# Optimization experiments

Measured on AMD Instinct MI355X. Metric: run time of the kernel, lower is better.

## Reference

```python
import jax, jax.numpy as jnp
import numpy as np

NEG_BIG = -9e15  # matches torch's -9000000000000000.0 mask value
ALPHA = 0.2      # LeakyReLU negative slope


def setup_inputs() -> dict:
    key = jax.random.key(0)
    k1, k2, k3 = jax.random.split(key, 3)
    B, N, Fin, Fout = 8, 2048, 64, 64
    h = jax.random.normal(k1, (B, N, Fin), dtype=jnp.float32)
    adj = jax.random.randint(k2, (B, N, N), 0, 2, dtype=jnp.int32)
    kW, ka = jax.random.split(k3)
    # xavier_uniform with gain=1.414
    gW = 1.414 * np.sqrt(6.0 / (Fin + Fout))
    W = jax.random.uniform(kW, (Fin, Fout), minval=-gW, maxval=gW, dtype=jnp.float32)
    ga = 1.414 * np.sqrt(6.0 / (2 * Fout + 1))
    a = jax.random.uniform(ka, (2 * Fout, 1), minval=-ga, maxval=ga, dtype=jnp.float32)
    return {"h": h, "adj": adj, "W": W, "a": a}


def reference(h, adj, W, a):
    # Wh: [B, N, Fout]
    Wh = jnp.einsum("bnf,fo->bno", h, W)
    Fout = W.shape[1]
    a1 = a[:Fout, 0]   # source part of attention vector
    a2 = a[Fout:, 0]   # target part
    # e_ij = leakyrelu(a1.Wh_i + a2.Wh_j) -- rank-1 decomposition of the
    # repeat/cat construction; avoids the [B,N,N,2F] intermediate.
    s = Wh @ a1        # [B, N]
    t = Wh @ a2        # [B, N]
    e = s[:, :, None] + t[:, None, :]            # [B, N, N]
    e = jnp.where(e > 0, e, ALPHA * e)           # LeakyReLU
    e = jnp.where(adj > 0, e, NEG_BIG)           # adjacency mask
    attention = jax.nn.softmax(e, axis=2)
    # dropout omitted: reference is eval-mode (F.dropout is identity when not training)
    h_prime = jnp.einsum("bij,bjo->bio", attention, Wh)
    return jax.nn.elu(h_prime)                   # concat=True branch
```

## Files before the change

kernel.cpp:

```cpp
#include <hip/hip_runtime.h>


#define ALPHA 0.2f

typedef __attribute__((ext_vector_type(8))) short  short8;
typedef __attribute__((ext_vector_type(4))) float  f32x4;

static __device__ __forceinline__ unsigned short f2bf(float f) {
    unsigned u = __builtin_bit_cast(unsigned, f);
    u += 0x7fffu + ((u >> 16) & 1u);
    return (unsigned short)(u >> 16);
}

static __device__ __forceinline__ unsigned pack_bf2(float lo, float hi) {
    unsigned ulo = __builtin_bit_cast(unsigned, lo) + 0x8000u;
    unsigned uhi = __builtin_bit_cast(unsigned, hi) + 0x8000u;
    return __builtin_amdgcn_perm(uhi, ulo, 0x07060302);
}

__global__ __launch_bounds__(256) void k01(
    const float* __restrict__ h, const int* __restrict__ adj,
    const float* __restrict__ W, const float* __restrict__ a,
    uint4* __restrict__ whF, float* __restrict__ sw,
    float* __restrict__ tw, unsigned char* __restrict__ mask)
{
    __shared__ float W_l[64 * 65];
    __shared__ float wa[128];
    __shared__ float tile[4 * 16 * 65];

    const int tid = threadIdx.x;

    if (blockIdx.x >= 256) {
        const int mb = blockIdx.x - 256;
        const int4* a4 = (const int4*)adj;
        #pragma unroll 1
        for (int g0 = 0; g0 < 16; g0 += 4) {
            int4 v0a, v0b, v1a, v1b, v2a, v2b, v3a, v3b;
            const size_t p0 = (size_t)mb * 4096 + (size_t)g0 * 256 + tid;
            v0a = a4[p0 * 2];          v0b = a4[p0 * 2 + 1];
            v1a = a4[(p0 + 256) * 2];  v1b = a4[(p0 + 256) * 2 + 1];
            v2a = a4[(p0 + 512) * 2];  v2b = a4[(p0 + 512) * 2 + 1];
            v3a = a4[(p0 + 768) * 2];  v3b = a4[(p0 + 768) * 2 + 1];
            unsigned b0 = (v0a.x ? 1u:0u)|(v0a.y ? 2u:0u)|(v0a.z ? 4u:0u)|(v0a.w ? 8u:0u)
                        | (v0b.x ?16u:0u)|(v0b.y ?32u:0u)|(v0b.z ?64u:0u)|(v0b.w ?128u:0u);
            unsigned b1 = (v1a.x ? 1u:0u)|(v1a.y ? 2u:0u)|(v1a.z ? 4u:0u)|(v1a.w ? 8u:0u)
                        | (v1b.x ?16u:0u)|(v1b.y ?32u:0u)|(v1b.z ?64u:0u)|(v1b.w ?128u:0u);
            unsigned b2 = (v2a.x ? 1u:0u)|(v2a.y ? 2u:0u)|(v2a.z ? 4u:0u)|(v2a.w ? 8u:0u)
                        | (v2b.x ?16u:0u)|(v2b.y ?32u:0u)|(v2b.z ?64u:0u)|(v2b.w ?128u:0u);
            unsigned b3 = (v3a.x ? 1u:0u)|(v3a.y ? 2u:0u)|(v3a.z ? 4u:0u)|(v3a.w ? 8u:0u)
                        | (v3b.x ?16u:0u)|(v3b.y ?32u:0u)|(v3b.z ?64u:0u)|(v3b.w ?128u:0u);
            mask[p0]       = (unsigned char)b0;
            mask[p0 + 256] = (unsigned char)b1;
            mask[p0 + 512] = (unsigned char)b2;
            mask[p0 + 768] = (unsigned char)b3;
        }
        return;
    }

    const int lane = tid & 63, wv = tid >> 6;
    const int im   = lane & 15, kq = lane >> 4;

    #pragma unroll
    for (int k = 0; k < 16; ++k) {
        int e = tid + 256 * k;
        W_l[(e >> 6) * 65 + (e & 63)] = W[e];
    }
    __syncthreads();

    if (tid < 128) {
        int f = tid & 63;
        const float* ap = a + (tid >> 6) * 64;
        float acc = 0.f;
        #pragma unroll 8
        for (int o = 0; o < 64; ++o) acc += W_l[f * 65 + o] * ap[o];
        wa[tid] = acc;
    }
    __syncthreads();

    short8 bf[4][2];
    #pragma unroll
    for (int nb = 0; nb < 4; ++nb)
        #pragma unroll
        for (int ks = 0; ks < 2; ++ks)
            #pragma unroll
            for (int u = 0; u < 8; ++u)
                bf[nb][ks][u] = (short)f2bf(W_l[(ks * 32 + kq * 8 + u) * 65 + nb * 16 + im]);

    const int row0 = blockIdx.x * 64 + wv * 16;
    const float* hrow = h + (size_t)(row0 + im) * 64;

    float hv[2][8];
    short8 af[2];
    float sp = 0.f, tp = 0.f;
    #pragma unroll
    for (int ks = 0; ks < 2; ++ks) {
        float4 A = *(const float4*)(hrow + ks * 32 + kq * 8);
        float4 Bv = *(const float4*)(hrow + ks * 32 + kq * 8 + 4);
        hv[ks][0] = A.x;  hv[ks][1] = A.y;  hv[ks][2] = A.z;  hv[ks][3] = A.w;
        hv[ks][4] = Bv.x; hv[ks][5] = Bv.y; hv[ks][6] = Bv.z; hv[ks][7] = Bv.w;
        #pragma unroll
        for (int u = 0; u < 8; ++u) {
            int f = ks * 32 + kq * 8 + u;
            sp += hv[ks][u] * wa[f];
            tp += hv[ks][u] * wa[64 + f];
            af[ks][u] = (short)f2bf(hv[ks][u]);
        }
    }
    sp += __shfl_xor(sp, 16, 64); sp += __shfl_xor(sp, 32, 64);
    tp += __shfl_xor(tp, 16, 64); tp += __shfl_xor(tp, 32, 64);
    if (lane < 16) {
        sw[row0 + lane] = sp;
        tw[row0 + lane] = tp;
    }

    f32x4 acc[4] = {{0.f,0.f,0.f,0.f},{0.f,0.f,0.f,0.f},{0.f,0.f,0.f,0.f},{0.f,0.f,0.f,0.f}};
    #pragma unroll
    for (int ks = 0; ks < 2; ++ks)
        #pragma unroll
        for (int nb = 0; nb < 4; ++nb)
            acc[nb] = __builtin_amdgcn_mfma_f32_16x16x32_bf16(af[ks], bf[nb][ks], acc[nb], 0, 0, 0);

    #pragma unroll
    for (int nb = 0; nb < 4; ++nb)
        #pragma unroll
        for (int r = 0; r < 4; ++r)
            tile[wv * 1040 + (kq * 4 + r) * 65 + nb * 16 + im] = acc[nb][r];
    __syncthreads();

    {
        const int blk_row0 = blockIdx.x * 64;
        const int bb2 = blk_row0 >> 11;
        const int c_base = (blk_row0 & 2047) >> 5;
        #pragma unroll
        for (int k = 0; k < 2; ++k) {
            int e = tid + 256 * k;
            int l = e & 63, ot = (e >> 6) & 3, cl_ = e >> 8;
            int o = ot * 16 + (l & 15);
            int jb = cl_ * 32 + (l >> 4) * 8;
            unsigned d0, d1, d2, d3;
            {
                int j0 = jb;
                d0 = pack_bf2(tile[(j0 >> 4) * 1040 + (j0 & 15) * 65 + o],
                              tile[(j0 >> 4) * 1040 + ((j0 & 15) + 1) * 65 + o]);
                j0 = jb + 2;
                d1 = pack_bf2(tile[(j0 >> 4) * 1040 + (j0 & 15) * 65 + o],
                              tile[(j0 >> 4) * 1040 + ((j0 & 15) + 1) * 65 + o]);
                j0 = jb + 4;
                d2 = pack_bf2(tile[(j0 >> 4) * 1040 + (j0 & 15) * 65 + o],
                              tile[(j0 >> 4) * 1040 + ((j0 & 15) + 1) * 65 + o]);
                j0 = jb + 6;
                d3 = pack_bf2(tile[(j0 >> 4) * 1040 + (j0 & 15) * 65 + o],
                              tile[(j0 >> 4) * 1040 + ((j0 & 15) + 1) * 65 + o]);
            }
            uint4 val = {d0, d1, d2, d3};
            whF[(size_t)(((bb2 * 64 + c_base + cl_) * 4 + ot)) * 64 + l] = val;
        }
    }
}

__global__ __launch_bounds__(256, 2) void k2_attn(
    const unsigned* __restrict__ mask, const uint4* __restrict__ whF,
    const float* __restrict__ sw, const float* __restrict__ tw,
    float* __restrict__ out)
{
    __shared__ float eB[2048];
    __shared__ float eD[2048];
    __shared__ float cpart[4 * 2176];

    const int tid  = threadIdx.x;
    const int lane = tid & 63, wv = tid >> 6;
    const int im   = lane & 15, kq = lane >> 4;
    const int b    = blockIdx.x >> 6;
    const int i0   = (blockIdx.x & 63) << 5;

    {
        const float4* tp4 = (const float4*)(tw + (size_t)b * 2048);
        float4 t0 = tp4[tid], t1 = tp4[tid + 256];
        float4 e0 = {__expf(t0.x), __expf(t0.y), __expf(t0.z), __expf(t0.w)};
        float4 e1 = {__expf(t1.x), __expf(t1.y), __expf(t1.z), __expf(t1.w)};
        float4 f0 = {__expf(ALPHA*t0.x), __expf(ALPHA*t0.y), __expf(ALPHA*t0.z), __expf(ALPHA*t0.w)};
        float4 f1 = {__expf(ALPHA*t1.x), __expf(ALPHA*t1.y), __expf(ALPHA*t1.z), __expf(ALPHA*t1.w)};
        *(float4*)&eB[tid * 4] = e0;  *(float4*)&eB[(tid + 256) * 4] = e1;
        *(float4*)&eD[tid * 4] = f0;  *(float4*)&eD[(tid + 256) * 4] = f1;
    }

    const uint4* mr0 = (const uint4*)(mask + (size_t)(b * 2048 + i0 + im) * 64 + wv * 16);
    const uint4* mr1 = (const uint4*)(mask + (size_t)(b * 2048 + i0 + 16 + im) * 64 + wv * 16);
    const uint4 mA0 = mr0[0], mB0 = mr0[1], mC0 = mr0[2], mD0 = mr0[3];
    const uint4 mA1 = mr1[0], mB1 = mr1[1], mC1 = mr1[2], mD1 = mr1[3];
    const unsigned mm0[16] = {mA0.x, mA0.y, mA0.z, mA0.w, mB0.x, mB0.y, mB0.z, mB0.w,
                              mC0.x, mC0.y, mC0.z, mC0.w, mD0.x, mD0.y, mD0.z, mD0.w};
    const unsigned mm1[16] = {mA1.x, mA1.y, mA1.z, mA1.w, mB1.x, mB1.y, mB1.z, mB1.w,
                              mC1.x, mC1.y, mC1.z, mC1.w, mD1.x, mD1.y, mD1.z, mD1.w};

    const float sl0 = sw[b * 2048 + i0 + im];
    const float sl1 = sw[b * 2048 + i0 + 16 + im];
    const float al0 = __expf(sl0), cl0 = __expf(ALPHA * sl0);
    const float al1 = __expf(sl1), cl1 = __expf(ALPHA * sl1);

    const int j00 = wv * 512 + kq * 8;
    const uint4* wbase = whF + (size_t)((b * 64 + wv * 16) * 4) * 64 + lane;

    short8 onesf;
    {
        const short ov = (im == 0) ? (short)0x3F80 : (short)0;
        #pragma unroll
        for (int u = 0; u < 8; ++u) onesf[u] = ov;
    }

    __syncthreads();

    f32x4 acc0 = {0.f,0.f,0.f,0.f}, acc1 = {0.f,0.f,0.f,0.f};
    f32x4 acc2 = {0.f,0.f,0.f,0.f}, acc3 = {0.f,0.f,0.f,0.f};
    f32x4 acc4 = {0.f,0.f,0.f,0.f}, acc5 = {0.f,0.f,0.f,0.f};
    f32x4 acc6 = {0.f,0.f,0.f,0.f}, acc7 = {0.f,0.f,0.f,0.f};
    f32x4 az0  = {0.f,0.f,0.f,0.f}, az1  = {0.f,0.f,0.f,0.f};

    #pragma unroll
    for (int s = 0; s < 16; ++s) {
        const uint4 w0 = wbase[(s * 4 + 0) * 64];
        const uint4 w1 = wbase[(s * 4 + 1) * 64];
        const uint4 w2 = wbase[(s * 4 + 2) * 64];
        const uint4 w3 = wbase[(s * 4 + 3) * 64];

        const float4 bA  = *(const float4*)&eB[j00 + s * 32];
        const float4 bBv = *(const float4*)&eB[j00 + s * 32 + 4];
        const float4 dA  = *(const float4*)&eD[j00 + s * 32];
        const float4 dBv = *(const float4*)&eD[j00 + s * 32 + 4];
        const unsigned mb0 = (mm0[s] >> (kq * 8)) & 0xffu;
        const unsigned mb1 = (mm1[s] >> (kq * 8)) & 0xffu;

        float p0 = fmaxf(al0 * bA.x,  cl0 * dA.x);   p0 = (mb0 &   1u) ? p0 : 0.f;
        float p1 = fmaxf(al0 * bA.y,  cl0 * dA.y);   p1 = (mb0 &   2u) ? p1 : 0.f;
        float p2 = fmaxf(al0 * bA.z,  cl0 * dA.z);   p2 = (mb0 &   4u) ? p2 : 0.f;
        float p3 = fmaxf(al0 * bA.w,  cl0 * dA.w);   p3 = (mb0 &   8u) ? p3 : 0.f;
        float p4 = fmaxf(al0 * bBv.x, cl0 * dBv.x);  p4 = (mb0 &  16u) ? p4 : 0.f;
        float p5 = fmaxf(al0 * bBv.y, cl0 * dBv.y);  p5 = (mb0 &  32u) ? p5 : 0.f;
        float p6 = fmaxf(al0 * bBv.z, cl0 * dBv.z);  p6 = (mb0 &  64u) ? p6 : 0.f;
        float p7 = fmaxf(al0 * bBv.w, cl0 * dBv.w);  p7 = (mb0 & 128u) ? p7 : 0.f;

        int4 ai0;
        ai0.x = (int)pack_bf2(p0, p1);
        ai0.y = (int)pack_bf2(p2, p3);
        ai0.z = (int)pack_bf2(p4, p5);
        ai0.w = (int)pack_bf2(p6, p7);
        const short8 af0 = __builtin_bit_cast(short8, ai0);

        float q0 = fmaxf(al1 * bA.x,  cl1 * dA.x);   q0 = (mb1 &   1u) ? q0 : 0.f;
        float q1 = fmaxf(al1 * bA.y,  cl1 * dA.y);   q1 = (mb1 &   2u) ? q1 : 0.f;
        float q2 = fmaxf(al1 * bA.z,  cl1 * dA.z);   q2 = (mb1 &   4u) ? q2 : 0.f;
        float q3 = fmaxf(al1 * bA.w,  cl1 * dA.w);   q3 = (mb1 &   8u) ? q3 : 0.f;
        float q4 = fmaxf(al1 * bBv.x, cl1 * dBv.x);  q4 = (mb1 &  16u) ? q4 : 0.f;
        float q5 = fmaxf(al1 * bBv.y, cl1 * dBv.y);  q5 = (mb1 &  32u) ? q5 : 0.f;
        float q6 = fmaxf(al1 * bBv.z, cl1 * dBv.z);  q6 = (mb1 &  64u) ? q6 : 0.f;
        float q7 = fmaxf(al1 * bBv.w, cl1 * dBv.w);  q7 = (mb1 & 128u) ? q7 : 0.f;

        int4 ai1;
        ai1.x = (int)pack_bf2(q0, q1);
        ai1.y = (int)pack_bf2(q2, q3);
        ai1.z = (int)pack_bf2(q4, q5);
        ai1.w = (int)pack_bf2(q6, q7);
        const short8 af1 = __builtin_bit_cast(short8, ai1);

        acc0 = __builtin_amdgcn_mfma_f32_16x16x32_bf16(af0, __builtin_bit_cast(short8, w0), acc0, 0, 0, 0);
        acc1 = __builtin_amdgcn_mfma_f32_16x16x32_bf16(af0, __builtin_bit_cast(short8, w1), acc1, 0, 0, 0);
        acc2 = __builtin_amdgcn_mfma_f32_16x16x32_bf16(af0, __builtin_bit_cast(short8, w2), acc2, 0, 0, 0);
        acc3 = __builtin_amdgcn_mfma_f32_16x16x32_bf16(af0, __builtin_bit_cast(short8, w3), acc3, 0, 0, 0);
        az0  = __builtin_amdgcn_mfma_f32_16x16x32_bf16(af0, onesf, az0, 0, 0, 0);

        acc4 = __builtin_amdgcn_mfma_f32_16x16x32_bf16(af1, __builtin_bit_cast(short8, w0), acc4, 0, 0, 0);
        acc5 = __builtin_amdgcn_mfma_f32_16x16x32_bf16(af1, __builtin_bit_cast(short8, w1), acc5, 0, 0, 0);
        acc6 = __builtin_amdgcn_mfma_f32_16x16x32_bf16(af1, __builtin_bit_cast(short8, w2), acc6, 0, 0, 0);
        acc7 = __builtin_amdgcn_mfma_f32_16x16x32_bf16(af1, __builtin_bit_cast(short8, w3), acc7, 0, 0, 0);
        az1  = __builtin_amdgcn_mfma_f32_16x16x32_bf16(af1, onesf, az1, 0, 0, 0);
    }

    #pragma unroll
    for (int r = 0; r < 4; ++r) {
        const int row = kq * 4 + r;
        float* cp0 = &cpart[wv * 2176 + row * 68];
        cp0[ 0 + im] = acc0[r];
        cp0[16 + im] = acc1[r];
        cp0[32 + im] = acc2[r];
        cp0[48 + im] = acc3[r];
        float* cp1 = &cpart[wv * 2176 + (16 + row) * 68];
        cp1[ 0 + im] = acc4[r];
        cp1[16 + im] = acc5[r];
        cp1[32 + im] = acc6[r];
        cp1[48 + im] = acc7[r];
        if (im == 0) { cp0[64] = az0[r]; cp1[64] = az1[r]; }
    }
    __syncthreads();

    #pragma unroll
    for (int k = 0; k < 2; ++k) {
        const int idx4 = tid + 256 * k;
        const int i  = idx4 >> 4;
        const int oc = (idx4 & 15) << 2;
        const float4 s0 = *(const float4*)&cpart[0 * 2176 + i * 68 + oc];
        const float4 s1 = *(const float4*)&cpart[1 * 2176 + i * 68 + oc];
        const float4 s2 = *(const float4*)&cpart[2 * 2176 + i * 68 + oc];
        const float4 s3 = *(const float4*)&cpart[3 * 2176 + i * 68 + oc];
        float z = cpart[0 * 2176 + i * 68 + 64] + cpart[1 * 2176 + i * 68 + 64]
                + cpart[2 * 2176 + i * 68 + 64] + cpart[3 * 2176 + i * 68 + 64];
        if (z == 0.f) z = 1.f;
        const float inv = 1.f / z;
        float4 rv;
        rv.x = ((s0.x + s1.x) + (s2.x + s3.x)) * inv;
        rv.y = ((s0.y + s1.y) + (s2.y + s3.y)) * inv;
        rv.z = ((s0.z + s1.z) + (s2.z + s3.z)) * inv;
        rv.w = ((s0.w + s1.w) + (s2.w + s3.w)) * inv;
        rv.x = rv.x > 0.f ? rv.x : expm1f(rv.x);
        rv.y = rv.y > 0.f ? rv.y : expm1f(rv.y);
        rv.z = rv.z > 0.f ? rv.z : expm1f(rv.z);
        rv.w = rv.w > 0.f ? rv.w : expm1f(rv.w);
        *(float4*)(out + ((size_t)(b * 2048 + i0 + i)) * 64 + oc) = rv;
    }
}

extern "C" void kernel_launch(void* const* d_in, const int* in_sizes, int n_in,
                              void* d_out, int out_size, void* d_ws, size_t ws_size,
                              hipStream_t stream) {
    const float* h   = (const float*)d_in[0];
    const int*   adj = (const int*)d_in[1];
    const float* W   = (const float*)d_in[2];
    const float* a   = (const float*)d_in[3];
    float* out = (float*)d_out;

    uint4* whF = (uint4*)d_ws;
    float* sw  = (float*)((char*)d_ws + 2097152);
    float* tw  = (float*)((char*)d_ws + 2097152 + 65536);
    unsigned char* mask = (unsigned char*)((char*)d_ws + 2097152 + 131072);

    hipLaunchKernelGGL(k01, dim3(1280), dim3(256), 0, stream, h, adj, W, a, whF, sw, tw, mask);
    hipLaunchKernelGGL(k2_attn, dim3(512), dim3(256), 0, stream,
                       (const unsigned*)mask, whF, sw, tw, out);
}
```

Measured before the change: 212.8 us.

## Read int32 adjacency directly in attention kernel, drop bitmask pre-pass

Removes the adjacency-to-bitmask compaction blocks from the first kernel, so it now only computes Wh, s and t. The attention kernel loads the int32 adjacency rows itself inside its main loop and uses them as the softmax mask. This drops the write and re-read of the intermediate bitmask and the extra blocks in the first launch. The cost is that the large adjacency read now happens inside the occupancy-limited attention kernel, with less coalesced 32-byte-per-lane row accesses. That could add memory latency to the compute loop.

Result: faster. 204.5 us (-3.9%).

```diff
diff --git a/kernel.cpp b/kernel.cpp
--- a/kernel.cpp
+++ b/kernel.cpp
@@ -18,45 +18,16 @@
     return __builtin_amdgcn_perm(uhi, ulo, 0x07060302);
 }
 
-__global__ __launch_bounds__(256) void k01(
-    const float* __restrict__ h, const int* __restrict__ adj,
-    const float* __restrict__ W, const float* __restrict__ a,
-    uint4* __restrict__ whF, float* __restrict__ sw,
-    float* __restrict__ tw, unsigned char* __restrict__ mask)
+__global__ __launch_bounds__(256) void k1(
+    const float* __restrict__ h, const float* __restrict__ W,
+    const float* __restrict__ a, uint4* __restrict__ whF,
+    float* __restrict__ sw, float* __restrict__ tw)
 {
     __shared__ float W_l[64 * 65];
     __shared__ float wa[128];
     __shared__ float tile[4 * 16 * 65];
 
     const int tid = threadIdx.x;
-
-    if (blockIdx.x >= 256) {
-        const int mb = blockIdx.x - 256;
-        const int4* a4 = (const int4*)adj;
-        #pragma unroll 1
-        for (int g0 = 0; g0 < 16; g0 += 4) {
-            int4 v0a, v0b, v1a, v1b, v2a, v2b, v3a, v3b;
-            const size_t p0 = (size_t)mb * 4096 + (size_t)g0 * 256 + tid;
-            v0a = a4[p0 * 2];          v0b = a4[p0 * 2 + 1];
-            v1a = a4[(p0 + 256) * 2];  v1b = a4[(p0 + 256) * 2 + 1];
-            v2a = a4[(p0 + 512) * 2];  v2b = a4[(p0 + 512) * 2 + 1];
-            v3a = a4[(p0 + 768) * 2];  v3b = a4[(p0 + 768) * 2 + 1];
-            unsigned b0 = (v0a.x ? 1u:0u)|(v0a.y ? 2u:0u)|(v0a.z ? 4u:0u)|(v0a.w ? 8u:0u)
-                        | (v0b.x ?16u:0u)|(v0b.y ?32u:0u)|(v0b.z ?64u:0u)|(v0b.w ?128u:0u);
-            unsigned b1 = (v1a.x ? 1u:0u)|(v1a.y ? 2u:0u)|(v1a.z ? 4u:0u)|(v1a.w ? 8u:0u)
-                        | (v1b.x ?16u:0u)|(v1b.y ?32u:0u)|(v1b.z ?64u:0u)|(v1b.w ?128u:0u);
-            unsigned b2 = (v2a.x ? 1u:0u)|(v2a.y ? 2u:0u)|(v2a.z ? 4u:0u)|(v2a.w ? 8u:0u)
-                        | (v2b.x ?16u:0u)|(v2b.y ?32u:0u)|(v2b.z ?64u:0u)|(v2b.w ?128u:0u);
-            unsigned b3 = (v3a.x ? 1u:0u)|(v3a.y ? 2u:0u)|(v3a.z ? 4u:0u)|(v3a.w ? 8u:0u)
-                        | (v3b.x ?16u:0u)|(v3b.y ?32u:0u)|(v3b.z ?64u:0u)|(v3b.w ?128u:0u);
-            mask[p0]       = (unsigned char)b0;
-            mask[p0 + 256] = (unsigned char)b1;
-            mask[p0 + 512] = (unsigned char)b2;
-            mask[p0 + 768] = (unsigned char)b3;
-        }
-        return;
-    }
-
     const int lane = tid & 63, wv = tid >> 6;
     const int im   = lane & 15, kq = lane >> 4;
 
@@ -159,7 +130,7 @@
 }
 
 __global__ __launch_bounds__(256, 2) void k2_attn(
-    const unsigned* __restrict__ mask, const uint4* __restrict__ whF,
+    const int* __restrict__ adj, const uint4* __restrict__ whF,
     const float* __restrict__ sw, const float* __restrict__ tw,
     float* __restrict__ out)
 {
@@ -184,21 +155,15 @@
         *(float4*)&eD[tid * 4] = f0;  *(float4*)&eD[(tid + 256) * 4] = f1;
     }
 
-    const uint4* mr0 = (const uint4*)(mask + (size_t)(b * 2048 + i0 + im) * 64 + wv * 16);
-    const uint4* mr1 = (const uint4*)(mask + (size_t)(b * 2048 + i0 + 16 + im) * 64 + wv * 16);
-    const uint4 mA0 = mr0[0], mB0 = mr0[1], mC0 = mr0[2], mD0 = mr0[3];
-    const uint4 mA1 = mr1[0], mB1 = mr1[1], mC1 = mr1[2], mD1 = mr1[3];
-    const unsigned mm0[16] = {mA0.x, mA0.y, mA0.z, mA0.w, mB0.x, mB0.y, mB0.z, mB0.w,
-                              mC0.x, mC0.y, mC0.z, mC0.w, mD0.x, mD0.y, mD0.z, mD0.w};
-    const unsigned mm1[16] = {mA1.x, mA1.y, mA1.z, mA1.w, mB1.x, mB1.y, mB1.z, mB1.w,
-                              mC1.x, mC1.y, mC1.z, mC1.w, mD1.x, mD1.y, mD1.z, mD1.w};
+    const int j00 = wv * 512 + kq * 8;
+    const int4* arow0 = (const int4*)(adj + (size_t)(b * 2048 + i0 + im) * 2048) + (j00 >> 2);
+    const int4* arow1 = (const int4*)(adj + (size_t)(b * 2048 + i0 + 16 + im) * 2048) + (j00 >> 2);
 
     const float sl0 = sw[b * 2048 + i0 + im];
     const float sl1 = sw[b * 2048 + i0 + 16 + im];
     const float al0 = __expf(sl0), cl0 = __expf(ALPHA * sl0);
     const float al1 = __expf(sl1), cl1 = __expf(ALPHA * sl1);
 
-    const int j00 = wv * 512 + kq * 8;
     const uint4* wbase = whF + (size_t)((b * 64 + wv * 16) * 4) * 64 + lane;
 
     short8 onesf;
@@ -223,21 +188,24 @@
         const uint4 w2 = wbase[(s * 4 + 2) * 64];
         const uint4 w3 = wbase[(s * 4 + 3) * 64];
 
+        const int4 a0A = arow0[s * 8];
+        const int4 a0B = arow0[s * 8 + 1];
+        const int4 a1A = arow1[s * 8];
+        const int4 a1B = arow1[s * 8 + 1];
+
         const float4 bA  = *(const float4*)&eB[j00 + s * 32];
         const float4 bBv = *(const float4*)&eB[j00 + s * 32 + 4];
         const float4 dA  = *(const float4*)&eD[j00 + s * 32];
         const float4 dBv = *(const float4*)&eD[j00 + s * 32 + 4];
-        const unsigned mb0 = (mm0[s] >> (kq * 8)) & 0xffu;
-        const unsigned mb1 = (mm1[s] >> (kq * 8)) & 0xffu;
-
-        float p0 = fmaxf(al0 * bA.x,  cl0 * dA.x);   p0 = (mb0 &   1u) ? p0 : 0.f;
-        float p1 = fmaxf(al0 * bA.y,  cl0 * dA.y);   p1 = (mb0 &   2u) ? p1 : 0.f;
-        float p2 = fmaxf(al0 * bA.z,  cl0 * dA.z);   p2 = (mb0 &   4u) ? p2 : 0.f;
-        float p3 = fmaxf(al0 * bA.w,  cl0 * dA.w);   p3 = (mb0 &   8u) ? p3 : 0.f;
-        float p4 = fmaxf(al0 * bBv.x, cl0 * dBv.x);  p4 = (mb0 &  16u) ? p4 : 0.f;
-        float p5 = fmaxf(al0 * bBv.y, cl0 * dBv.y);  p5 = (mb0 &  32u) ? p5 : 0.f;
-        float p6 = fmaxf(al0 * bBv.z, cl0 * dBv.z);  p6 = (mb0 &  64u) ? p6 : 0.f;
-        float p7 = fmaxf(al0 * bBv.w, cl0 * dBv.w);  p7 = (mb0 & 128u) ? p7 : 0.f;
+
+        float p0 = fmaxf(al0 * bA.x,  cl0 * dA.x);   p0 = a0A.x ? p0 : 0.f;
+        float p1 = fmaxf(al0 * bA.y,  cl0 * dA.y);   p1 = a0A.y ? p1 : 0.f;
+        float p2 = fmaxf(al0 * bA.z,  cl0 * dA.z);   p2 = a0A.z ? p2 : 0.f;
+        float p3 = fmaxf(al0 * bA.w,  cl0 * dA.w);   p3 = a0A.w ? p3 : 0.f;
+        float p4 = fmaxf(al0 * bBv.x, cl0 * dBv.x);  p4 = a0B.x ? p4 : 0.f;
+        float p5 = fmaxf(al0 * bBv.y, cl0 * dBv.y);  p5 = a0B.y ? p5 : 0.f;
+        float p6 = fmaxf(al0 * bBv.z, cl0 * dBv.z);  p6 = a0B.z ? p6 : 0.f;
+        float p7 = fmaxf(al0 * bBv.w, cl0 * dBv.w);  p7 = a0B.w ? p7 : 0.f;
 
         int4 ai0;
         ai0.x = (int)pack_bf2(p0, p1);
@@ -246,14 +214,14 @@
         ai0.w = (int)pack_bf2(p6, p7);
         const short8 af0 = __builtin_bit_cast(short8, ai0);
 
-        float q0 = fmaxf(al1 * bA.x,  cl1 * dA.x);   q0 = (mb1 &   1u) ? q0 : 0.f;
-        float q1 = fmaxf(al1 * bA.y,  cl1 * dA.y);   q1 = (mb1 &   2u) ? q1 : 0.f;
-        float q2 = fmaxf(al1 * bA.z,  cl1 * dA.z);   q2 = (mb1 &   4u) ? q2 : 0.f;
-        float q3 = fmaxf(al1 * bA.w,  cl1 * dA.w);   q3 = (mb1 &   8u) ? q3 : 0.f;
-        float q4 = fmaxf(al1 * bBv.x, cl1 * dBv.x);  q4 = (mb1 &  16u) ? q4 : 0.f;
-        float q5 = fmaxf(al1 * bBv.y, cl1 * dBv.y);  q5 = (mb1 &  32u) ? q5 : 0.f;
-        float q6 = fmaxf(al1 * bBv.z, cl1 * dBv.z);  q6 = (mb1 &  64u) ? q6 : 0.f;
-        float q7 = fmaxf(al1 * bBv.w, cl1 * dBv.w);  q7 = (mb1 & 128u) ? q7 : 0.f;
+        float q0 = fmaxf(al1 * bA.x,  cl1 * dA.x);   q0 = a1A.x ? q0 : 0.f;
+        float q1 = fmaxf(al1 * bA.y,  cl1 * dA.y);   q1 = a1A.y ? q1 : 0.f;
+        float q2 = fmaxf(al1 * bA.z,  cl1 * dA.z);   q2 = a1A.z ? q2 : 0.f;
+        float q3 = fmaxf(al1 * bA.w,  cl1 * dA.w);   q3 = a1A.w ? q3 : 0.f;
+        float q4 = fmaxf(al1 * bBv.x, cl1 * dBv.x);  q4 = a1B.x ? q4 : 0.f;
+        float q5 = fmaxf(al1 * bBv.y, cl1 * dBv.y);  q5 = a1B.y ? q5 : 0.f;
+        float q6 = fmaxf(al1 * bBv.z, cl1 * dBv.z);  q6 = a1B.z ? q6 : 0.f;
+        float q7 = fmaxf(al1 * bBv.w, cl1 * dBv.w);  q7 = a1B.w ? q7 : 0.f;
 
         int4 ai1;
         ai1.x = (int)pack_bf2(q0, q1);
@@ -330,9 +298,8 @@
     uint4* whF = (uint4*)d_ws;
     float* sw  = (float*)((char*)d_ws + 2097152);
     float* tw  = (float*)((char*)d_ws + 2097152 + 65536);
-    unsigned char* mask = (unsigned char*)((char*)d_ws + 2097152 + 131072);
-
-    hipLaunchKernelGGL(k01, dim3(1280), dim3(256), 0, stream, h, adj, W, a, whF, sw, tw, mask);
+
+    hipLaunchKernelGGL(k1, dim3(256), dim3(256), 0, stream, h, W, a, whF, sw, tw);
     hipLaunchKernelGGL(k2_attn, dim3(512), dim3(256), 0, stream,
-                       (const unsigned*)mask, whF, sw, tw, out);
-}
+                       adj, whF, sw, tw, out);
+}
```
